# Kernel optimization log

Measured on AMD Instinct MI355X. Metric: run time of the kernel, lower is better.

## Reference

```python
import jax, jax.numpy as jnp
import numpy as np

M, IN_F, OUT_F = 16384, 2048, 2048

def sign_fn(x):
    # torch.sign(torch.sign(x) + 0.5): maps 0 -> +1, otherwise +/-1
    return jnp.sign(jnp.sign(x) + 0.5)

def setup_inputs() -> dict:
    key = jax.random.key(0)
    kx, kw = jax.random.split(key)
    # Upstream BNN activations are binary +/-1 (required for the packed-bit
    # backward in the original module to be exact).
    x = sign_fn(jax.random.normal(kx, (M, IN_F), dtype=jnp.float32))
    weight = jax.random.uniform(kw, (OUT_F, IN_F), dtype=jnp.float32) * 0.01
    return {"x": x, "weight": weight}

def reference(x, weight):
    # xnor=False path: SignFunctionNoSTE -> binarize weight, then dense matmul
    b_weight = sign_fn(weight)          # [OUT_F, IN_F], values in {-1, +1}
    return x @ b_weight.T               # [M, OUT_F]
```

## Files before the change

### kernel.cpp

```cpp
#include <hip/hip_runtime.h>
#include <stdint.h>

typedef unsigned long long u64;

#define M_DIM 16384
#define N_DIM 2048
#define K_DIM 2048

#define BM 128
#define BN 256
#define BK 64
#define NSTAGE (K_DIM / BK)

typedef int v4i  __attribute__((ext_vector_type(4)));
typedef int v16i __attribute__((ext_vector_type(16)));


__device__ __forceinline__ void gld16(void* lds_base, const void* gsrc) {
    __builtin_amdgcn_global_load_lds(
        (const __attribute__((address_space(1))) uint32_t*)gsrc,
        (__attribute__((address_space(3))) uint32_t*)lds_base,
        16, 0, 0);
}

__device__ __forceinline__ int pk4(float a, float b, float c, float d) {
    int r = (a < 0.0f ? 0xFF : 0x01);
    r |= (b < 0.0f ? 0xFF : 0x01) << 8;
    r |= (c < 0.0f ? 0xFF : 0x01) << 16;
    r |= (d < 0.0f ? 0xFF : 0x01) << 24;
    return r;
}

template <int T>
__global__ __launch_bounds__(256) void pack_i8_kernel(
        const float* __restrict__ src, char* __restrict__ dst) {
    const int wave_id = (blockIdx.x * 256 + threadIdx.x) >> 6;
    const int lane = threadIdx.x & 63;
    const int s  = wave_id & (NSTAGE - 1);
    const int rg = wave_id >> 5;
    const int r  = lane & 31;
    const int kh = lane >> 5;
    const int regs = 2 * T;
    char* out = dst + ((size_t)rg * NSTAGE + s) * (regs * 1024) + lane * 16;
#pragma unroll 2
    for (int rr = 0; rr < regs; ++rr) {
        const int c = rr / T, t = rr % T;
        const int row = rg * (T * 32) + t * 32 + r;
        const float* p = src + (size_t)row * K_DIM + s * BK + c * 32 + kh * 16;
        const float4 v0 = ((const float4*)p)[0];
        const float4 v1 = ((const float4*)p)[1];
        const float4 v2 = ((const float4*)p)[2];
        const float4 v3 = ((const float4*)p)[3];
        int4 o;
        o.x = pk4(v0.x, v0.y, v0.z, v0.w);
        o.y = pk4(v1.x, v1.y, v1.z, v1.w);
        o.z = pk4(v2.x, v2.y, v2.z, v2.w);
        o.w = pk4(v3.x, v3.y, v3.z, v3.w);
        *(int4*)(out + rr * 1024) = o;
    }
}

__global__ __launch_bounds__(256, 2) void bgemm_i8_kernel(
        const char* __restrict__ Ap, const char* __restrict__ Bp,
        float* __restrict__ C) {
    __shared__ __align__(16) char As[8 * 1024];
    __shared__ __align__(16) char Bs[16 * 1024];

    const int t    = threadIdx.x;
    const int lane = t & 63;
    const int wv   = t >> 6;
    const int m_blk = blockIdx.y;
    const int n_blk = blockIdx.x;

    const int wm = (wv >> 1) * 2;
    const int wn = (wv & 1) * 4;

    const char* aS = Ap + (size_t)m_blk * (NSTAGE * 8192);
    const char* bS = Bp + (size_t)n_blk * (NSTAGE * 16384);

    v16i acc[2][4];
#pragma unroll
    for (int i = 0; i < 2; ++i)
#pragma unroll
        for (int j = 0; j < 4; ++j)
#pragma unroll
            for (int q = 0; q < 16; ++q) acc[i][j][q] = 0;

    const int wv6 = wv * 6;
    for (int s = 0; s < NSTAGE; ++s) {
#pragma unroll
        for (int r = 0; r < 6; ++r) {
            const int reg = wv6 + r;
            const bool isA = reg < 8;
            const char* g = isA ? (aS + reg * 1024) : (bS + (reg - 8) * 1024);
            char* l = isA ? (As + reg * 1024) : (Bs + (reg - 8) * 1024);
            gld16(l, g + lane * 16);
        }
        aS += 8192;
        bS += 16384;
        __syncthreads();

#pragma unroll
        for (int c = 0; c < 2; ++c) {
            v4i af[2], bf[4];
#pragma unroll
            for (int i = 0; i < 2; ++i)
                af[i] = *(const v4i*)(As + (c * 4 + wm + i) * 1024 + lane * 16);
#pragma unroll
            for (int j = 0; j < 4; ++j)
                bf[j] = *(const v4i*)(Bs + (c * 8 + wn + j) * 1024 + lane * 16);
#pragma unroll
            for (int i = 0; i < 2; ++i)
#pragma unroll
                for (int j = 0; j < 4; ++j)
                    acc[i][j] = __builtin_amdgcn_mfma_i32_32x32x32_i8(
                        af[i], bf[j], acc[i][j], 0, 0, 0);
        }
        __syncthreads();
    }

    const int col = lane & 31;
    const int rq  = (lane >> 5) * 4;
#pragma unroll
    for (int i = 0; i < 2; ++i) {
#pragma unroll
        for (int j = 0; j < 4; ++j) {
            const int mbase = m_blk * BM + (wm + i) * 32;
            const int nbase = n_blk * BN + (wn + j) * 32;
#pragma unroll
            for (int q = 0; q < 16; ++q) {
                const int row = mbase + (q & 3) + 8 * (q >> 2) + rq;
                C[(size_t)row * N_DIM + nbase + col] = (float)acc[i][j][q];
            }
        }
    }
}

#define KC 32
#define KT 16
struct alignas(16) u64x2 { u64 x, y; };

__global__ __launch_bounds__(256) void pack_sign_kernel(
        const float* __restrict__ in, u64* __restrict__ out, int ngroups) {
    int wid  = (blockIdx.x * 256 + threadIdx.x) >> 6;
    int lane = threadIdx.x & 63;
    if (wid >= ngroups) return;
    const float4* p = reinterpret_cast<const float4*>(in) + (size_t)wid * 64 + lane;
    float4 v = *p;
    u64 b0 = __ballot(v.x < 0.0f);
    u64 b1 = __ballot(v.y < 0.0f);
    u64 b2 = __ballot(v.z < 0.0f);
    u64 b3 = __ballot(v.w < 0.0f);
    if (lane == 0) {
        u64* o = out + (size_t)wid * 4;
        o[0] = b0; o[1] = b1; o[2] = b2; o[3] = b3;
    }
}

__global__ __launch_bounds__(256, 2) void bgemm_kernel(
        const u64* __restrict__ A, const u64* __restrict__ B,
        float* __restrict__ C) {
    __shared__ u64 As[KT][128];
    __shared__ u64 Bs[KT][128];
    const int t     = threadIdx.x;
    const int m_blk = blockIdx.y << 7;
    const int n_blk = blockIdx.x << 7;
    const int lane = t & 63;
    const int wave = t >> 6;
    const int tm   = lane >> 3;
    const int tn   = lane & 7;
    const int m0   = ((wave >> 1) << 6) + (tm << 3);
    const int n0   = ((wave & 1) << 6) + (tn << 3);
    unsigned acc[8][8];
#pragma unroll
    for (int i = 0; i < 8; ++i)
#pragma unroll
        for (int j = 0; j < 8; ++j) acc[i][j] = 0u;
    const int sr = t >> 3;
    const int sc = (t << 1) & 15;
    for (int ks = 0; ks < K_DIM / (KT * 64); ++ks) {
        const int cbase = ks * KT;
#pragma unroll
        for (int i = 0; i < 4; ++i) {
            int r = i * 32 + sr;
            u64x2 va = *reinterpret_cast<const u64x2*>(A + (size_t)(m_blk + r) * KC + cbase + sc);
            As[sc][r] = va.x; As[sc + 1][r] = va.y;
            u64x2 vb = *reinterpret_cast<const u64x2*>(B + (size_t)(n_blk + r) * KC + cbase + sc);
            Bs[sc][r] = vb.x; Bs[sc + 1][r] = vb.y;
        }
        __syncthreads();
#pragma unroll 1
        for (int c = 0; c < KT; ++c) {
            u64 a[8], b[8];
#pragma unroll
            for (int i = 0; i < 4; ++i) {
                u64x2 va = *reinterpret_cast<const u64x2*>(&As[c][m0 + 2 * i]);
                a[2 * i] = va.x; a[2 * i + 1] = va.y;
                u64x2 vb = *reinterpret_cast<const u64x2*>(&Bs[c][n0 + 2 * i]);
                b[2 * i] = vb.x; b[2 * i + 1] = vb.y;
            }
#pragma unroll
            for (int i = 0; i < 8; ++i)
#pragma unroll
                for (int j = 0; j < 8; ++j)
                    acc[i][j] += (unsigned)__builtin_popcountll(a[i] ^ b[j]);
        }
        __syncthreads();
    }
#pragma unroll
    for (int i = 0; i < 8; ++i) {
        float* o = C + (size_t)(m_blk + m0 + i) * N_DIM + n_blk + n0;
        float4 v0, v1;
        v0.x = (float)(K_DIM - 2 * (int)acc[i][0]);
        v0.y = (float)(K_DIM - 2 * (int)acc[i][1]);
        v0.z = (float)(K_DIM - 2 * (int)acc[i][2]);
        v0.w = (float)(K_DIM - 2 * (int)acc[i][3]);
        v1.x = (float)(K_DIM - 2 * (int)acc[i][4]);
        v1.y = (float)(K_DIM - 2 * (int)acc[i][5]);
        v1.z = (float)(K_DIM - 2 * (int)acc[i][6]);
        v1.w = (float)(K_DIM - 2 * (int)acc[i][7]);
        *reinterpret_cast<float4*>(o)     = v0;
        *reinterpret_cast<float4*>(o + 4) = v1;
    }
}

extern "C" void kernel_launch(void* const* d_in, const int* in_sizes, int n_in,
                              void* d_out, int out_size, void* d_ws, size_t ws_size,
                              hipStream_t stream) {
    const float* x = (const float*)d_in[0];
    const float* w = (const float*)d_in[1];
    float* out = (float*)d_out;

    const size_t needA = (size_t)M_DIM * K_DIM;
    const size_t needB = (size_t)N_DIM * K_DIM;
    if (ws_size >= needA + needB) {
        char* Ap = (char*)d_ws;
        char* Bp = Ap + needA;
        pack_i8_kernel<4><<<4096 / 4, 256, 0, stream>>>(x, Ap);
        pack_i8_kernel<8><<<256 / 4, 256, 0, stream>>>(w, Bp);
        bgemm_i8_kernel<<<dim3(N_DIM / BN, M_DIM / BM), 256, 0, stream>>>(Ap, Bp, out);
    } else {
        u64* xb = (u64*)d_ws;
        u64* wb = xb + (size_t)M_DIM * KC;
        int xgroups = (M_DIM * K_DIM) / 256;
        int wgroups = (N_DIM * K_DIM) / 256;
        pack_sign_kernel<<<xgroups / 4, 256, 0, stream>>>(x, xb, xgroups);
        pack_sign_kernel<<<wgroups / 4, 256, 0, stream>>>(w, wb, wgroups);
        bgemm_kernel<<<dim3(N_DIM / 128, M_DIM / 128), 256, 0, stream>>>(xb, wb, out);
    }
}
```

Before: 329.9 us.

## Load MFMA fragments directly from global with register double-buffering and XCD remap

Drops the LDS staging and the block barriers from the int8 MFMA GEMM. Each wave now loads its pre-packed fragments straight from global memory into registers, double-buffered so the next stage's loads overlap the current MFMAs. It also switches to a 1D grid remapped so each XCD works on a contiguous band of M blocks, aiming for better L2 reuse. The cost is that waves sharing a tile no longer share loads, so global and L2 traffic goes up, and register pressure rises.

Result: slower. 338.9 us (+2.7%).

```diff
diff --git a/kernel.cpp b/kernel.cpp
--- a/kernel.cpp
+++ b/kernel.cpp
@@ -15,13 +15,6 @@
 typedef int v4i  __attribute__((ext_vector_type(4)));
 typedef int v16i __attribute__((ext_vector_type(16)));
 
-
-__device__ __forceinline__ void gld16(void* lds_base, const void* gsrc) {
-    __builtin_amdgcn_global_load_lds(
-        (const __attribute__((address_space(1))) uint32_t*)gsrc,
-        (__attribute__((address_space(3))) uint32_t*)lds_base,
-        16, 0, 0);
-}
 
 __device__ __forceinline__ int pk4(float a, float b, float c, float d) {
     int r = (a < 0.0f ? 0xFF : 0x01);
@@ -60,23 +53,43 @@
     }
 }
 
+struct Frags {
+    v4i a[2][2];
+    v4i b[2][4];
+};
+
+__device__ __forceinline__ void load_frags(
+        Frags& f, const char* __restrict__ aS, const char* __restrict__ bS,
+        int wm, int wn) {
+#pragma unroll
+    for (int c = 0; c < 2; ++c) {
+#pragma unroll
+        for (int i = 0; i < 2; ++i)
+            f.a[c][i] = *(const v4i*)(aS + (c * 4 + wm + i) * 1024);
+#pragma unroll
+        for (int j = 0; j < 4; ++j)
+            f.b[c][j] = *(const v4i*)(bS + (c * 8 + wn + j) * 1024);
+    }
+}
+
 __global__ __launch_bounds__(256, 2) void bgemm_i8_kernel(
         const char* __restrict__ Ap, const char* __restrict__ Bp,
         float* __restrict__ C) {
-    __shared__ __align__(16) char As[8 * 1024];
-    __shared__ __align__(16) char Bs[16 * 1024];
-
     const int t    = threadIdx.x;
     const int lane = t & 63;
     const int wv   = t >> 6;
-    const int m_blk = blockIdx.y;
-    const int n_blk = blockIdx.x;
+
+    const int id    = blockIdx.x;
+    const int xcd   = id & 7;
+    const int idx   = id >> 3;
+    const int m_blk = xcd * 16 + (idx & 15);
+    const int n_blk = idx >> 4;
 
     const int wm = (wv >> 1) * 2;
     const int wn = (wv & 1) * 4;
 
-    const char* aS = Ap + (size_t)m_blk * (NSTAGE * 8192);
-    const char* bS = Bp + (size_t)n_blk * (NSTAGE * 16384);
+    const char* aS = Ap + (size_t)m_blk * (NSTAGE * 8192)  + lane * 16;
+    const char* bS = Bp + (size_t)n_blk * (NSTAGE * 16384) + lane * 16;
 
     v16i acc[2][4];
 #pragma unroll
@@ -86,37 +99,28 @@
 #pragma unroll
             for (int q = 0; q < 16; ++q) acc[i][j][q] = 0;
 
-    const int wv6 = wv * 6;
-    for (int s = 0; s < NSTAGE; ++s) {
-#pragma unroll
-        for (int r = 0; r < 6; ++r) {
-            const int reg = wv6 + r;
-            const bool isA = reg < 8;
-            const char* g = isA ? (aS + reg * 1024) : (bS + (reg - 8) * 1024);
-            char* l = isA ? (As + reg * 1024) : (Bs + (reg - 8) * 1024);
-            gld16(l, g + lane * 16);
-        }
-        aS += 8192;
-        bS += 16384;
-        __syncthreads();
-
-#pragma unroll
-        for (int c = 0; c < 2; ++c) {
-            v4i af[2], bf[4];
-#pragma unroll
-            for (int i = 0; i < 2; ++i)
-                af[i] = *(const v4i*)(As + (c * 4 + wm + i) * 1024 + lane * 16);
-#pragma unroll
-            for (int j = 0; j < 4; ++j)
-                bf[j] = *(const v4i*)(Bs + (c * 8 + wn + j) * 1024 + lane * 16);
+    auto compute = [&](const Frags& f) {
+#pragma unroll
+        for (int c = 0; c < 2; ++c)
 #pragma unroll
             for (int i = 0; i < 2; ++i)
 #pragma unroll
                 for (int j = 0; j < 4; ++j)
                     acc[i][j] = __builtin_amdgcn_mfma_i32_32x32x32_i8(
-                        af[i], bf[j], acc[i][j], 0, 0, 0);
-        }
-        __syncthreads();
+                        f.a[c][i], f.b[c][j], acc[i][j], 0, 0, 0);
+    };
+
+    Frags f0, f1;
+    load_frags(f0, aS, bS, wm, wn);
+#pragma unroll 1
+    for (int s = 0; s < NSTAGE; s += 2) {
+        load_frags(f1, aS + (size_t)(s + 1) * 8192,
+                        bS + (size_t)(s + 1) * 16384, wm, wn);
+        compute(f0);
+        if (s + 2 < NSTAGE)
+            load_frags(f0, aS + (size_t)(s + 2) * 8192,
+                            bS + (size_t)(s + 2) * 16384, wm, wn);
+        compute(f1);
     }
 
     const int col = lane & 31;
@@ -238,7 +242,7 @@
         char* Bp = Ap + needA;
         pack_i8_kernel<4><<<4096 / 4, 256, 0, stream>>>(x, Ap);
         pack_i8_kernel<8><<<256 / 4, 256, 0, stream>>>(w, Bp);
-        bgemm_i8_kernel<<<dim3(N_DIM / BN, M_DIM / BM), 256, 0, stream>>>(Ap, Bp, out);
+        bgemm_i8_kernel<<<(M_DIM / BM) * (N_DIM / BN), 256, 0, stream>>>(Ap, Bp, out);
     } else {
         u64* xb = (u64*)d_ws;
         u64* wb = xb + (size_t)M_DIM * KC;
```

## Double-buffer LDS, enlarge GEMM tile to 256x256, remap blocks per XCD

Applied to the files above, without the earlier changes.

The int8 MFMA GEMM moves to 512-thread blocks with a 256x256 output tile. The A packing is changed to match the larger row group. LDS is double-buffered so the async global-to-LDS load of the next K stage is issued before computing the current one, leaving a single barrier per stage. Blocks are launched on a 1D grid and remapped so that consecutive ids on the same XCD share M tiles, aiming for better L2 reuse. The cost is 64KB of LDS per block, which may limit occupancy.

After: 318.8 us. 3.4% less time.

```diff
diff --git a/kernel.cpp b/kernel.cpp
--- a/kernel.cpp
+++ b/kernel.cpp
@@ -7,7 +7,7 @@
 #define N_DIM 2048
 #define K_DIM 2048
 
-#define BM 128
+#define BM 256
 #define BN 256
 #define BK 64
 #define NSTAGE (K_DIM / BK)
@@ -60,23 +60,25 @@
     }
 }
 
-__global__ __launch_bounds__(256, 2) void bgemm_i8_kernel(
+__global__ __launch_bounds__(512, 2) void bgemm_i8_kernel(
         const char* __restrict__ Ap, const char* __restrict__ Bp,
         float* __restrict__ C) {
-    __shared__ __align__(16) char As[8 * 1024];
-    __shared__ __align__(16) char Bs[16 * 1024];
+    __shared__ __align__(16) char lds[2][32 * 1024];
 
     const int t    = threadIdx.x;
     const int lane = t & 63;
     const int wv   = t >> 6;
-    const int m_blk = blockIdx.y;
-    const int n_blk = blockIdx.x;
-
-    const int wm = (wv >> 1) * 2;
-    const int wn = (wv & 1) * 4;
-
-    const char* aS = Ap + (size_t)m_blk * (NSTAGE * 8192);
-    const char* bS = Bp + (size_t)n_blk * (NSTAGE * 16384);
+    const int wm   = (wv >> 1) & 3;
+    const int wn   = wv & 1;
+
+    const int id    = blockIdx.x;
+    const int xcd   = id & 7;
+    const int idx   = id >> 3;
+    const int m_blk = xcd * 8 + (idx & 7);
+    const int n_blk = idx >> 3;
+
+    const char* aG = Ap + (size_t)m_blk * (NSTAGE * 16384);
+    const char* bG = Bp + (size_t)n_blk * (NSTAGE * 16384);
 
     v16i acc[2][4];
 #pragma unroll
@@ -86,29 +88,30 @@
 #pragma unroll
             for (int q = 0; q < 16; ++q) acc[i][j][q] = 0;
 
-    const int wv6 = wv * 6;
-    for (int s = 0; s < NSTAGE; ++s) {
-#pragma unroll
-        for (int r = 0; r < 6; ++r) {
-            const int reg = wv6 + r;
-            const bool isA = reg < 8;
-            const char* g = isA ? (aS + reg * 1024) : (bS + (reg - 8) * 1024);
-            char* l = isA ? (As + reg * 1024) : (Bs + (reg - 8) * 1024);
-            gld16(l, g + lane * 16);
-        }
-        aS += 8192;
-        bS += 16384;
-        __syncthreads();
-
+    auto dma = [&](int s, int buf) {
+        const char* a = aG + (size_t)s * 16384;
+        const char* b = bG + (size_t)s * 16384;
+#pragma unroll
+        for (int r = 0; r < 4; ++r) {
+            const int reg = wv * 4 + r;
+            const char* g = (reg < 16) ? (a + reg * 1024)
+                                       : (b + (reg - 16) * 1024);
+            gld16(&lds[buf][reg * 1024], g + lane * 16);
+        }
+    };
+
+    auto compute = [&](int buf) {
+        const char* As = lds[buf];
+        const char* Bs = lds[buf] + 16384;
 #pragma unroll
         for (int c = 0; c < 2; ++c) {
             v4i af[2], bf[4];
 #pragma unroll
             for (int i = 0; i < 2; ++i)
-                af[i] = *(const v4i*)(As + (c * 4 + wm + i) * 1024 + lane * 16);
+                af[i] = *(const v4i*)(As + (c * 8 + wm * 2 + i) * 1024 + lane * 16);
 #pragma unroll
             for (int j = 0; j < 4; ++j)
-                bf[j] = *(const v4i*)(Bs + (c * 8 + wn + j) * 1024 + lane * 16);
+                bf[j] = *(const v4i*)(Bs + (c * 8 + wn * 4 + j) * 1024 + lane * 16);
 #pragma unroll
             for (int i = 0; i < 2; ++i)
 #pragma unroll
@@ -116,6 +119,14 @@
                     acc[i][j] = __builtin_amdgcn_mfma_i32_32x32x32_i8(
                         af[i], bf[j], acc[i][j], 0, 0, 0);
         }
+    };
+
+    dma(0, 0);
+    __syncthreads();
+#pragma unroll 1
+    for (int s = 0; s < NSTAGE; ++s) {
+        if (s + 1 < NSTAGE) dma(s + 1, (s + 1) & 1);
+        compute(s & 1);
         __syncthreads();
     }
 
@@ -125,8 +136,8 @@
     for (int i = 0; i < 2; ++i) {
 #pragma unroll
         for (int j = 0; j < 4; ++j) {
-            const int mbase = m_blk * BM + (wm + i) * 32;
-            const int nbase = n_blk * BN + (wn + j) * 32;
+            const int mbase = m_blk * BM + (wm * 2 + i) * 32;
+            const int nbase = n_blk * BN + (wn * 4 + j) * 32;
 #pragma unroll
             for (int q = 0; q < 16; ++q) {
                 const int row = mbase + (q & 3) + 8 * (q >> 2) + rq;
@@ -236,9 +247,9 @@
     if (ws_size >= needA + needB) {
         char* Ap = (char*)d_ws;
         char* Bp = Ap + needA;
-        pack_i8_kernel<4><<<4096 / 4, 256, 0, stream>>>(x, Ap);
+        pack_i8_kernel<8><<<2048 / 4, 256, 0, stream>>>(x, Ap);
         pack_i8_kernel<8><<<256 / 4, 256, 0, stream>>>(w, Bp);
-        bgemm_i8_kernel<<<dim3(N_DIM / BN, M_DIM / BM), 256, 0, stream>>>(Ap, Bp, out);
+        bgemm_i8_kernel<<<(M_DIM / BM) * (N_DIM / BN), 512, 0, stream>>>(Ap, Bp, out);
     } else {
         u64* xb = (u64*)d_ws;
         u64* wb = xb + (size_t)M_DIM * KC;
```
